# Kernel optimization log

Measured on AMD Instinct MI355X. Metric: run time of the kernel, lower is better.

Reference implementation:

```python
import jax, jax.numpy as jnp
import numpy as np

K = 25          # moving-average kernel_size
P = 24          # periodicity
PAD_LEN = 5     # median padding window (padding_mode='median')


def setup_inputs() -> dict:
    key = jax.random.key(0)
    x = jax.random.normal(key, (64, 128, 8192), dtype=jnp.float32)
    return {"x": x}


def _decompose(x):
    B, C, L = x.shape
    half = (K - 1) // 2  # 12

    # --- moving_average_decomposition with 'median' padding ---
    # torch.median over an odd window (5) == jnp.median
    front = jnp.median(x[:, :, :PAD_LEN], axis=2, keepdims=True)   # [B,C,1]
    end = jnp.median(x[:, :, -PAD_LEN:], axis=2, keepdims=True)    # [B,C,1]
    xp = jnp.concatenate(
        [jnp.repeat(front, half, axis=2), x, jnp.repeat(end, half, axis=2)],
        axis=2,
    )  # [B,C,L+K-1]

    # AvgPool1d(kernel=K, stride=1) via prefix-sum difference (single pass)
    cs = jnp.cumsum(xp, axis=-1)
    cs = jnp.concatenate([jnp.zeros_like(cs[:, :, :1]), cs], axis=-1)
    trend = (cs[:, :, K:] - cs[:, :, :-K]) / K                      # [B,C,L]
    res = x - trend

    # --- per-phase seasonal mean (vectorized replacement of python loop) ---
    pad_len = L % P
    if pad_len > 0:
        # original: cat(res, res[:, :, -P:-pad_len]) -> length divisible by P
        xpad = jnp.concatenate([res, res[:, :, -P:-pad_len]], axis=-1)
    else:
        xpad = res
    n = xpad.shape[-1] // P
    # mean over occurrences of each phase i (== mean of x_padded[:, :, i::P])
    seasonal = jnp.mean(xpad.reshape(B, C, n, P), axis=2)           # [B,C,P]
    out_seasonal = jnp.tile(seasonal, (1, 1, n))[:, :, :L]          # broadcast back
    out_residual = res - out_seasonal
    return out_residual, trend, out_seasonal


def reference(x):
    return _decompose(x)
```

## Files before the change

### kernel.cpp

```cpp
#include <hip/hip_runtime.h>

namespace {
constexpr int LROW   = 8192;
constexpr int KWIN   = 25;
constexpr int HALF   = (KWIN - 1) / 2;
constexpr int PERIOD = 24;
constexpr int NOCC   = 342;
constexpr int NTHR   = 256;
constexpr int GRP    = LROW / (4 * NTHR);
}

__device__ __forceinline__ void ce(float& x, float& y) {
    float lo = fminf(x, y), hi = fmaxf(x, y);
    x = lo; y = hi;
}

__device__ __forceinline__ float median5(float a, float b, float c, float d, float e) {
    ce(a, b); ce(d, e); ce(c, e); ce(c, d); ce(a, d); ce(a, c);
    ce(b, e); ce(b, d); ce(b, c);
    return c;
}

__global__ __launch_bounds__(NTHR, 5) void decomp_kernel(
    const float* __restrict__ x,
    float* __restrict__ out_res,
    float* __restrict__ out_trend,
    float* __restrict__ out_seas)
{
    __shared__ __align__(16) float xs[LROW];

    const int t = threadIdx.x;
    const size_t base = (size_t)blockIdx.x * LROW;
    const float* xr = x + base;

    #pragma unroll
    for (int j = 0; j < GRP; ++j) {
        int g = 4 * (t + NTHR * j);
        *reinterpret_cast<float4*>(xs + g) =
            *reinterpret_cast<const float4*>(xr + g);
    }
    __syncthreads();

    float resv[GRP][4];
    #pragma unroll
    for (int j = 0; j < GRP; ++j) {
        int g = 4 * (t + NTHR * j);
        float v[28];
        if (g >= HALF && g <= LROW - 16) {
            #pragma unroll
            for (int q = 0; q < 7; ++q) {
                float4 f = *reinterpret_cast<const float4*>(xs + g - HALF + 4 * q);
                v[4*q+0] = f.x; v[4*q+1] = f.y; v[4*q+2] = f.z; v[4*q+3] = f.w;
            }
        } else {
            float med = (g < HALF)
                ? median5(xs[0], xs[1], xs[2], xs[3], xs[4])
                : median5(xs[LROW-5], xs[LROW-4], xs[LROW-3], xs[LROW-2], xs[LROW-1]);
            #pragma unroll
            for (int q = 0; q < 28; ++q) {
                int idx = g - HALF + q;
                v[q] = (idx < 0 || idx >= LROW) ? med : xs[idx];
            }
        }
        float s = 0.f;
        #pragma unroll
        for (int q = 0; q < KWIN; ++q) s += v[q];
        constexpr float inv = 1.0f / (float)KWIN;
        float w1 = s  - v[0] + v[25];
        float w2 = w1 - v[1] + v[26];
        float w3 = w2 - v[2] + v[27];
        float t0 = s * inv, t1 = w1 * inv, t2 = w2 * inv, t3 = w3 * inv;
        resv[j][0] = v[12] - t0;
        resv[j][1] = v[13] - t1;
        resv[j][2] = v[14] - t2;
        resv[j][3] = v[15] - t3;
        *reinterpret_cast<float4*>(out_trend + base + g) =
            make_float4(t0, t1, t2, t3);
    }
    __syncthreads();

    #pragma unroll
    for (int j = 0; j < GRP; ++j) {
        int g = 4 * (t + NTHR * j);
        *reinterpret_cast<float4*>(xs + g) =
            make_float4(resv[j][0], resv[j][1], resv[j][2], resv[j][3]);
    }
    __syncthreads();

    float acc = 0.f;
    if (t < 240) {
        const int p = t / 10, s0 = t % 10;
        for (int k = s0; k < NOCC; k += 10) {
            int m = PERIOD * k + p;
            if (m >= LROW) m -= PERIOD;
            acc += xs[m];
        }
    }
    __syncthreads();
    if (t < 240) xs[t] = acc;
    __syncthreads();
    if (t < PERIOD) {
        float s = 0.f;
        #pragma unroll
        for (int q = 0; q < 10; ++q) s += xs[t * 10 + q];
        xs[240 + t] = s / (float)NOCC;
    }
    __syncthreads();

    #pragma unroll
    for (int j = 0; j < GRP; ++j) {
        int g = 4 * (t + NTHR * j);
        int ph = g % PERIOD;
        float4 sv = *reinterpret_cast<const float4*>(xs + 240 + ph);
        *reinterpret_cast<float4*>(out_seas + base + g) = sv;
        *reinterpret_cast<float4*>(out_res + base + g) =
            make_float4(resv[j][0] - sv.x, resv[j][1] - sv.y,
                        resv[j][2] - sv.z, resv[j][3] - sv.w);
    }
}

extern "C" void kernel_launch(void* const* d_in, const int* in_sizes, int n_in,
                              void* d_out, int out_size, void* d_ws, size_t ws_size,
                              hipStream_t stream) {
    const float* x = (const float*)d_in[0];
    float* out = (float*)d_out;
    const size_t n = (size_t)in_sizes[0];
    const int rows = (int)(n / (size_t)LROW);
    decomp_kernel<<<rows, NTHR, 0, stream>>>(x, out, out + n, out + 2 * n);
}
```

Baseline: 211.3 us.

## Process several rows per block with double-buffered async global-to-LDS staging

Each block now handles 16 rows instead of one. The next rows' inputs are prefetched into a second LDS buffer with `__builtin_amdgcn_global_load_lds`, so those loads overlap the current row's compute and stores. The aim is to hide global load latency and cut per-block launch and setup overhead in this memory-bound kernel. In exchange, LDS per block doubles, occupancy drops to two blocks per CU, and the grid shrinks to 512 blocks, which may leave less parallelism to hide memory latency.

```diff
diff --git a/kernel.cpp b/kernel.cpp
--- a/kernel.cpp
+++ b/kernel.cpp
@@ -1,4 +1,5 @@
 #include <hip/hip_runtime.h>
+#include <cstdint>
 
 namespace {
 constexpr int LROW   = 8192;
@@ -8,6 +9,7 @@
 constexpr int NOCC   = 342;
 constexpr int NTHR   = 256;
 constexpr int GRP    = LROW / (4 * NTHR);
+constexpr int RPB    = 16;
 }
 
 __device__ __forceinline__ void ce(float& x, float& y) {
@@ -21,101 +23,127 @@
     return c;
 }
 
-__global__ __launch_bounds__(NTHR, 5) void decomp_kernel(
+__device__ __forceinline__ void stage_row(const float* __restrict__ xr,
+                                          float* ldsbuf, int t) {
+    #pragma unroll
+    for (int j = 0; j < GRP; ++j) {
+        int g = 4 * (t + NTHR * j);
+        __builtin_amdgcn_global_load_lds(
+            (const __attribute__((address_space(1))) uint32_t*)(xr + g),
+            (__attribute__((address_space(3))) uint32_t*)(ldsbuf + g),
+            16, 0, 0);
+    }
+}
+
+__global__ __launch_bounds__(NTHR, 2) void decomp_kernel(
     const float* __restrict__ x,
     float* __restrict__ out_res,
     float* __restrict__ out_trend,
     float* __restrict__ out_seas)
 {
-    __shared__ __align__(16) float xs[LROW];
+    __shared__ __align__(16) float buf[2][LROW];
+    __shared__ float part[240];
+    __shared__ float seasonal[PERIOD];
 
     const int t = threadIdx.x;
-    const size_t base = (size_t)blockIdx.x * LROW;
-    const float* xr = x + base;
+    const int b = blockIdx.x;
+    const int rstride = gridDim.x;
 
-    #pragma unroll
-    for (int j = 0; j < GRP; ++j) {
-        int g = 4 * (t + NTHR * j);
-        *reinterpret_cast<float4*>(xs + g) =
-            *reinterpret_cast<const float4*>(xr + g);
-    }
+    auto row_base = [&](int i) -> size_t {
+        return ((size_t)(b + i * rstride)) * (size_t)LROW;
+    };
+
+    stage_row(x + row_base(0), buf[0], t);
+    stage_row(x + row_base(1), buf[1], t);
     __syncthreads();
 
-    float resv[GRP][4];
-    #pragma unroll
-    for (int j = 0; j < GRP; ++j) {
-        int g = 4 * (t + NTHR * j);
-        float v[28];
-        if (g >= HALF && g <= LROW - 16) {
+    for (int i = 0; i < RPB; ++i) {
+        const int cur = i & 1;
+        const size_t base = row_base(i);
+        float* xs = buf[cur];
+
+        float resv[GRP][4];
+        #pragma unroll
+        for (int j = 0; j < GRP; ++j) {
+            int g = 4 * (t + NTHR * j);
+            float v[28];
+            if (g >= HALF && g <= LROW - 16) {
+                #pragma unroll
+                for (int q = 0; q < 7; ++q) {
+                    float4 f = *reinterpret_cast<const float4*>(xs + g - HALF + 4 * q);
+                    v[4*q+0] = f.x; v[4*q+1] = f.y; v[4*q+2] = f.z; v[4*q+3] = f.w;
+                }
+            } else {
+                float med = (g < HALF)
+                    ? median5(xs[0], xs[1], xs[2], xs[3], xs[4])
+                    : median5(xs[LROW-5], xs[LROW-4], xs[LROW-3], xs[LROW-2], xs[LROW-1]);
+                #pragma unroll
+                for (int q = 0; q < 28; ++q) {
+                    int idx = g - HALF + q;
+                    v[q] = (idx < 0 || idx >= LROW) ? med : xs[idx];
+                }
+            }
+            float s = 0.f;
             #pragma unroll
-            for (int q = 0; q < 7; ++q) {
-                float4 f = *reinterpret_cast<const float4*>(xs + g - HALF + 4 * q);
-                v[4*q+0] = f.x; v[4*q+1] = f.y; v[4*q+2] = f.z; v[4*q+3] = f.w;
+            for (int q = 0; q < KWIN; ++q) s += v[q];
+            constexpr float inv = 1.0f / (float)KWIN;
+            float w1 = s  - v[0] + v[25];
+            float w2 = w1 - v[1] + v[26];
+            float w3 = w2 - v[2] + v[27];
+            float t0 = s * inv, t1 = w1 * inv, t2 = w2 * inv, t3 = w3 * inv;
+            resv[j][0] = v[12] - t0;
+            resv[j][1] = v[13] - t1;
+            resv[j][2] = v[14] - t2;
+            resv[j][3] = v[15] - t3;
+            *reinterpret_cast<float4*>(out_trend + base + g) =
+                make_float4(t0, t1, t2, t3);
+        }
+        __syncthreads();
+
+        #pragma unroll
+        for (int j = 0; j < GRP; ++j) {
+            int g = 4 * (t + NTHR * j);
+            *reinterpret_cast<float4*>(xs + g) =
+                make_float4(resv[j][0], resv[j][1], resv[j][2], resv[j][3]);
+        }
+        __syncthreads();
+
+        if (t < 240) {
+            const int p = t / 10, s0 = t % 10;
+            float acc = 0.f;
+            for (int k = s0; k < NOCC; k += 10) {
+                int m = PERIOD * k + p;
+                if (m >= LROW) m -= PERIOD;
+                acc += xs[m];
             }
-        } else {
-            float med = (g < HALF)
-                ? median5(xs[0], xs[1], xs[2], xs[3], xs[4])
-                : median5(xs[LROW-5], xs[LROW-4], xs[LROW-3], xs[LROW-2], xs[LROW-1]);
+            part[t] = acc;
+        }
+        __syncthreads();
+
+        if (i + 2 < RPB) stage_row(x + row_base(i + 2), buf[cur], t);
+
+        if (t < PERIOD) {
+            float s = 0.f;
             #pragma unroll
-            for (int q = 0; q < 28; ++q) {
-                int idx = g - HALF + q;
-                v[q] = (idx < 0 || idx >= LROW) ? med : xs[idx];
-            }
+            for (int q = 0; q < 10; ++q) s += part[t * 10 + q];
+            seasonal[t] = s / (float)NOCC;
         }
-        float s = 0.f;
+        __syncthreads();
+
         #pragma unroll
-        for (int q = 0; q < KWIN; ++q) s += v[q];
-        constexpr float inv = 1.0f / (float)KWIN;
-        float w1 = s  - v[0] + v[25];
-        float w2 = w1 - v[1] + v[26];
-        float w3 = w2 - v[2] + v[27];
-        float t0 = s * inv, t1 = w1 * inv, t2 = w2 * inv, t3 = w3 * inv;
-        resv[j][0] = v[12] - t0;
-        resv[j][1] = v[13] - t1;
-        resv[j][2] = v[14] - t2;
-        resv[j][3] = v[15] - t3;
-        *reinterpret_cast<float4*>(out_trend + base + g) =
-            make_float4(t0, t1, t2, t3);
-    }
-    __syncthreads();
-
-    #pragma unroll
-    for (int j = 0; j < GRP; ++j) {
-        int g = 4 * (t + NTHR * j);
-        *reinterpret_cast<float4*>(xs + g) =
-            make_float4(resv[j][0], resv[j][1], resv[j][2], resv[j][3]);
-    }
-    __syncthreads();
-
-    float acc = 0.f;
-    if (t < 240) {
-        const int p = t / 10, s0 = t % 10;
-        for (int k = s0; k < NOCC; k += 10) {
-            int m = PERIOD * k + p;
-            if (m >= LROW) m -= PERIOD;
-            acc += xs[m];
+        for (int j = 0; j < GRP; ++j) {
+            int g = 4 * (t + NTHR * j);
+            int ph = g % PERIOD;
+            float s0 = seasonal[ph + 0];
+            float s1 = seasonal[ph + 1];
+            float s2 = seasonal[ph + 2];
+            float s3 = seasonal[ph + 3];
+            *reinterpret_cast<float4*>(out_seas + base + g) =
+                make_float4(s0, s1, s2, s3);
+            *reinterpret_cast<float4*>(out_res + base + g) =
+                make_float4(resv[j][0] - s0, resv[j][1] - s1,
+                            resv[j][2] - s2, resv[j][3] - s3);
         }
-    }
-    __syncthreads();
-    if (t < 240) xs[t] = acc;
-    __syncthreads();
-    if (t < PERIOD) {
-        float s = 0.f;
-        #pragma unroll
-        for (int q = 0; q < 10; ++q) s += xs[t * 10 + q];
-        xs[240 + t] = s / (float)NOCC;
-    }
-    __syncthreads();
-
-    #pragma unroll
-    for (int j = 0; j < GRP; ++j) {
-        int g = 4 * (t + NTHR * j);
-        int ph = g % PERIOD;
-        float4 sv = *reinterpret_cast<const float4*>(xs + 240 + ph);
-        *reinterpret_cast<float4*>(out_seas + base + g) = sv;
-        *reinterpret_cast<float4*>(out_res + base + g) =
-            make_float4(resv[j][0] - sv.x, resv[j][1] - sv.y,
-                        resv[j][2] - sv.z, resv[j][3] - sv.w);
     }
 }
 
@@ -126,5 +154,6 @@
     float* out = (float*)d_out;
     const size_t n = (size_t)in_sizes[0];
     const int rows = (int)(n / (size_t)LROW);
-    decomp_kernel<<<rows, NTHR, 0, stream>>>(x, out, out + n, out + 2 * n);
+    const int nblk = rows / RPB;
+    decomp_kernel<<<nblk, NTHR, 0, stream>>>(x, out, out + n, out + 2 * n);
 }
```

Measured after the change: 226.4 us. 7.1% more time.
